# Kernel optimization log

Measured on AMD Instinct MI355X. Metric: run time of the kernel, lower is better.

Reference implementation:

```python
import jax, jax.numpy as jnp
import numpy as np

# segment-boundary byte set (matches ByteContextEncoder.SEGMENT_BYTES)
_SEG_BYTES = b' \t\n\r.,;:!?()[]{}"\'' + b'+-*/=<>|&^~%@#$\\'
_SEP_TABLE = np.zeros(256, dtype=bool)
_SEP_TABLE[list(_SEG_BYTES)] = True

B, T, D, H, L = 4, 2048, 512, 8, 4
HID = 4 * D          # SwiGLU hidden dim
DH = D // H          # head dim
EPS = 1e-6
ALPHA = 0.5
ROPE_BASE = 10000.0


def setup_inputs() -> dict:
    key = jax.random.key(0)
    ks = jax.random.split(key, 10)
    std = D ** -0.5
    tokens = jax.random.randint(ks[0], (B, T), 0, 256)
    embed = jax.random.normal(ks[1], (256, D), dtype=jnp.float32) * std
    wq = jax.random.normal(ks[2], (L, D, D), dtype=jnp.float32) * std
    wk = jax.random.normal(ks[3], (L, D, D), dtype=jnp.float32) * std
    wv = jax.random.normal(ks[4], (L, D, D), dtype=jnp.float32) * std
    wo = jax.random.normal(ks[5], (L, D, D), dtype=jnp.float32) * std
    w1 = jax.random.normal(ks[6], (L, HID, D), dtype=jnp.float32) * std  # gate proj
    w3 = jax.random.normal(ks[7], (L, HID, D), dtype=jnp.float32) * std  # up proj
    w2 = jax.random.normal(ks[8], (L, D, HID), dtype=jnp.float32) * (HID ** -0.5)  # down proj
    attn_norm_w = jnp.ones((L, D), dtype=jnp.float32)
    ffn_norm_w = jnp.ones((L, D), dtype=jnp.float32)
    final_norm_w = jnp.ones((D,), dtype=jnp.float32)
    return {"tokens": tokens, "embed": embed, "attn_norm_w": attn_norm_w,
            "wq": wq, "wk": wk, "wv": wv, "wo": wo,
            "ffn_norm_w": ffn_norm_w, "w1": w1, "w2": w2, "w3": w3,
            "final_norm_w": final_norm_w}


def _rmsnorm(x, w):
    return x * jax.lax.rsqrt(jnp.mean(x * x, axis=-1, keepdims=True) + EPS) * w


def _rope_tables():
    inv = 1.0 / (ROPE_BASE ** (jnp.arange(0, DH, 2, dtype=jnp.float32) / DH))  # (DH/2,)
    ang = jnp.arange(T, dtype=jnp.float32)[:, None] * inv[None, :]             # (T, DH/2)
    return jnp.cos(ang), jnp.sin(ang)


def _apply_rope(x, cos, sin):
    # x: (B, T, H, DH); rotate interleaved pairs
    x1, x2 = x[..., ::2], x[..., 1::2]
    c = cos[None, :, None, :]
    s = sin[None, :, None, :]
    r1 = x1 * c - x2 * s
    r2 = x1 * s + x2 * c
    return jnp.stack([r1, r2], axis=-1).reshape(x.shape)


def _attention(x, Wq, Wk, Wv, Wo, cos, sin):
    q = (x @ Wq.T).reshape(B, T, H, DH)
    k = (x @ Wk.T).reshape(B, T, H, DH)
    v = (x @ Wv.T).reshape(B, T, H, DH)
    q = _apply_rope(q, cos, sin)
    k = _apply_rope(k, cos, sin)
    scores = jnp.einsum('bthd,bshd->bhts', q, k) / jnp.sqrt(jnp.float32(DH))
    a = jax.nn.softmax(scores, axis=-1)  # bidirectional (causal=False)
    o = jnp.einsum('bhts,bshd->bthd', a, v).reshape(B, T, D)
    return o @ Wo.T


def _swiglu(x, W1, W2, W3):
    return (jax.nn.silu(x @ W1.T) * (x @ W3.T)) @ W2.T


def _segment_pool(h, tokens):
    # segment ids via cumsum of separator indicator; per-batch offset b*(T+1)
    sep = jnp.asarray(_SEP_TABLE)[tokens].astype(jnp.int32)          # (B, T)
    seg = jnp.cumsum(sep, axis=1) + jnp.arange(B, dtype=jnp.int32)[:, None] * (T + 1)
    flat_s = seg.reshape(B * T)
    flat_h = h.reshape(B * T, D)
    nseg = B * (T + 1)
    seg_sum = jax.ops.segment_sum(flat_h, flat_s, num_segments=nseg)  # (nseg, D)
    seg_cnt = jax.ops.segment_sum(jnp.ones((B * T,), h.dtype), flat_s, num_segments=nseg)
    seg_cnt = jnp.maximum(seg_cnt, 1.0)
    seg_mean = (seg_sum / seg_cnt[:, None])[flat_s].reshape(B, T, D)
    return ALPHA * h + (1.0 - ALPHA) * seg_mean


def reference(tokens, embed, attn_norm_w, wq, wk, wv, wo, ffn_norm_w, w1, w2, w3, final_norm_w):
    tokens = jnp.clip(tokens, 0, 255)
    x = embed[tokens]  # (B, T, D); dropout=0 -> identity
    cos, sin = _rope_tables()
    for l in range(L):
        x = x + _attention(_rmsnorm(x, attn_norm_w[l]), wq[l], wk[l], wv[l], wo[l], cos, sin)
        x = x + _swiglu(_rmsnorm(x, ffn_norm_w[l]), w1[l], w2[l], w3[l])
    x = _rmsnorm(x, final_norm_w)
    return _segment_pool(x, tokens)
```

## Files before the change

kernel.cpp:

```cpp
#include <hip/hip_runtime.h>
#include <math.h>

#define Bq 4
#define Tt 2048
#define Dd 512
#define Hh 8
#define Ll 4
#define HIDN 2048
#define DHd 64
#define BT (Bq*Tt)
#define BTD ((size_t)BT*Dd)

typedef __attribute__((ext_vector_type(8))) __bf16 bf16x8;
typedef __attribute__((ext_vector_type(4))) __bf16 bf16x4;
typedef __attribute__((ext_vector_type(2))) __bf16 bf16x2;
typedef __attribute__((ext_vector_type(4))) float f32x4;

static __device__ __forceinline__ int is_sep(int t) {
    const unsigned long long w0 = 0xFC00FFFF00002600ULL;
    const unsigned long long w1 = 0x7800000078000001ULL;
    if (t < 64)  return (int)((w0 >> t) & 1ULL);
    if (t < 128) return (int)((w1 >> (t - 64)) & 1ULL);
    return 0;
}

static __device__ __forceinline__ void gload16(const void* g, void* l) {
    __builtin_amdgcn_global_load_lds(
        (const __attribute__((address_space(1))) void*)g,
        (__attribute__((address_space(3))) void*)l, 16, 0, 0);
}

__global__ void embed_kernel(const int* __restrict__ tokens, const float* __restrict__ embed,
                             float* __restrict__ x) {
    size_t idx = (size_t)blockIdx.x * blockDim.x + threadIdx.x;
    if (idx >= BTD / 4) return;
    size_t row = idx >> 7;
    int tk = tokens[row];
    tk = tk < 0 ? 0 : (tk > 255 ? 255 : tk);
    const float4* src = (const float4*)(embed + (size_t)tk * Dd);
    ((float4*)x)[idx] = src[idx & 127];
}

__global__ void rope_table_kernel(float* __restrict__ cosb, float* __restrict__ sinb) {
    int idx = blockIdx.x * blockDim.x + threadIdx.x;
    if (idx >= Tt * 32) return;
    int t = idx >> 5, j = idx & 31;
    float inv = powf(10000.0f, -(2.0f * j) / 64.0f);
    float ang = (float)t * inv;
    cosb[idx] = cosf(ang);
    sinb[idx] = sinf(ang);
}

__global__ void cvt_w_kernel(const float* __restrict__ wo, const float* __restrict__ w1,
                             const float* __restrict__ w3, const float* __restrict__ w2,
                             __bf16* __restrict__ dst) {
    int i = blockIdx.x * blockDim.x + threadIdx.x;
    if (i >= 1703936) return;
    const float* src;
    if (i < 131072)       src = wo + (size_t)i * 8;
    else if (i < 655360)  src = w1 + (size_t)(i - 131072) * 8;
    else if (i < 1179648) src = w3 + (size_t)(i - 655360) * 8;
    else                  src = w2 + (size_t)(i - 1179648) * 8;
    float4 a = *(const float4*)src;
    float4 b = *(const float4*)(src + 4);
    bf16x8 o8;
    o8[0] = (__bf16)a.x; o8[1] = (__bf16)a.y; o8[2] = (__bf16)a.z; o8[3] = (__bf16)a.w;
    o8[4] = (__bf16)b.x; o8[5] = (__bf16)b.y; o8[6] = (__bf16)b.z; o8[7] = (__bf16)b.w;
    *(bf16x8*)(dst + (size_t)i * 8) = o8;
}

__global__ void cvt_qkv_kernel(const float* __restrict__ wq, const float* __restrict__ wk,
                               const float* __restrict__ wv, __bf16* __restrict__ out) {
    int i = blockIdx.x * blockDim.x + threadIdx.x;
    if (i >= 393216) return;
    int l = i / 98304;
    int r = i - l * 98304;
    int t = r >> 15;
    int pos8 = r & 32767;
    const float* src = (t == 0 ? wq : (t == 1 ? wk : wv)) + (size_t)l * 262144 + (size_t)pos8 * 8;
    float4 a = *(const float4*)src;
    float4 b = *(const float4*)(src + 4);
    bf16x8 o8;
    o8[0] = (__bf16)a.x; o8[1] = (__bf16)a.y; o8[2] = (__bf16)a.z; o8[3] = (__bf16)a.w;
    o8[4] = (__bf16)b.x; o8[5] = (__bf16)b.y; o8[6] = (__bf16)b.z; o8[7] = (__bf16)b.w;
    *(bf16x8*)(out + (size_t)i * 8) = o8;
}

__global__ void rmsnorm_bf16_kernel(const float* __restrict__ x, const float* __restrict__ w,
                                    __bf16* __restrict__ y) {
    int row = blockIdx.x * 4 + (threadIdx.x >> 6);
    int lane = threadIdx.x & 63;
    const float* xr = x + (size_t)row * Dd + lane * 8;
    float4 a = *(const float4*)xr;
    float4 b = *(const float4*)(xr + 4);
    float ss = a.x * a.x + a.y * a.y + a.z * a.z + a.w * a.w
             + b.x * b.x + b.y * b.y + b.z * b.z + b.w * b.w;
    #pragma unroll
    for (int off = 1; off < 64; off <<= 1) ss += __shfl_xor(ss, off);
    float scale = rsqrtf(ss * (1.0f / Dd) + 1e-6f);
    const float* wr = w + lane * 8;
    float4 wa = *(const float4*)wr;
    float4 wb = *(const float4*)(wr + 4);
    bf16x8 o;
    o[0] = (__bf16)(a.x * scale * wa.x); o[1] = (__bf16)(a.y * scale * wa.y);
    o[2] = (__bf16)(a.z * scale * wa.z); o[3] = (__bf16)(a.w * scale * wa.w);
    o[4] = (__bf16)(b.x * scale * wb.x); o[5] = (__bf16)(b.y * scale * wb.y);
    o[6] = (__bf16)(b.z * scale * wb.z); o[7] = (__bf16)(b.w * scale * wb.w);
    *(bf16x8*)(y + (size_t)row * Dd + lane * 8) = o;
}

__global__ void rmsnorm_inplace_kernel(float* __restrict__ x, const float* __restrict__ w) {
    int row = blockIdx.x * 4 + (threadIdx.x >> 6);
    int lane = threadIdx.x & 63;
    float* xr = x + (size_t)row * Dd + lane * 8;
    float4 a = *(const float4*)xr;
    float4 b = *(const float4*)(xr + 4);
    float ss = a.x * a.x + a.y * a.y + a.z * a.z + a.w * a.w
             + b.x * b.x + b.y * b.y + b.z * b.z + b.w * b.w;
    #pragma unroll
    for (int off = 1; off < 64; off <<= 1) ss += __shfl_xor(ss, off);
    float scale = rsqrtf(ss * (1.0f / Dd) + 1e-6f);
    const float* wr = w + lane * 8;
    float4 wa = *(const float4*)wr;
    float4 wb = *(const float4*)(wr + 4);
    *(float4*)xr = make_float4(a.x * scale * wa.x, a.y * scale * wa.y,
                               a.z * scale * wa.z, a.w * scale * wa.w);
    *(float4*)(xr + 4) = make_float4(b.x * scale * wb.x, b.y * scale * wb.y,
                                     b.z * scale * wb.z, b.w * scale * wb.w);
}

template<int EPI>
__global__ __launch_bounds__(256) void gemm_bt_mfma(
    const __bf16* __restrict__ A, const __bf16* __restrict__ Bw,
    const float* __restrict__ res, void* __restrict__ Cout,
    int N, int K,
    const float* __restrict__ cosb, const float* __restrict__ sinb) {
    __shared__ __align__(16) __bf16 lds[2][2][128 * 32];
    const int tid = threadIdx.x;
    const int w = tid >> 6, lane = tid & 63;
    const int l15 = lane & 15, g4 = lane >> 4;
    const int wr = w >> 1, wc = w & 1;
    const int bm = blockIdx.y * 128, bn = blockIdx.x * 128;
    const int lrow = lane >> 2, lc8 = (lane & 3) * 8;
    const int chunk0 = w * 2;

    f32x4 acc[4][4];
    #pragma unroll
    for (int m = 0; m < 4; m++)
        #pragma unroll
        for (int n = 0; n < 4; n++) acc[m][n] = (f32x4){0.f, 0.f, 0.f, 0.f};

    auto stage = [&](int buf, int k0) {
        #pragma unroll
        for (int c = 0; c < 2; c++) {
            int chunk = chunk0 + c;
            const __bf16* ga = A + (size_t)(bm + chunk * 16 + lrow) * K + k0 + lc8;
            gload16(ga, &lds[buf][0][chunk * 512]);
            const __bf16* gb = Bw + (size_t)(bn + chunk * 16 + lrow) * K + k0 + lc8;
            gload16(gb, &lds[buf][1][chunk * 512]);
        }
    };

    stage(0, 0);
    __syncthreads();
    const int NT = K >> 5;
    int cur = 0;
    for (int t = 0; t < NT; t++) {
        if (t + 1 < NT) stage(cur ^ 1, (t + 1) << 5);
        const __bf16* Al = &lds[cur][0][0];
        const __bf16* Bl = &lds[cur][1][0];
        bf16x8 af[4], bfr[4];
        #pragma unroll
        for (int m = 0; m < 4; m++)
            af[m] = *(const bf16x8*)&Al[(wr * 64 + m * 16 + l15) * 32 + g4 * 8];
        #pragma unroll
        for (int n = 0; n < 4; n++)
            bfr[n] = *(const bf16x8*)&Bl[(wc * 64 + n * 16 + l15) * 32 + g4 * 8];
        #pragma unroll
        for (int m = 0; m < 4; m++)
            #pragma unroll
            for (int n = 0; n < 4; n++)
                acc[m][n] = __builtin_amdgcn_mfma_f32_16x16x32_bf16(af[m], bfr[n], acc[m][n], 0, 0, 0);
        __syncthreads();
        cur ^= 1;
    }

    #pragma unroll
    for (int m = 0; m < 4; m++)
        #pragma unroll
        for (int n = 0; n < 4; n++)
            #pragma unroll
            for (int r = 0; r < 4; r++) {
                size_t row = bm + wr * 64 + m * 16 + g4 * 4 + r;
                int col = bn + wc * 64 + n * 16 + l15;
                if (EPI == 0) {
                    ((__bf16*)Cout)[row * N + col] = (__bf16)acc[m][n][r];
                } else if (EPI == 1) {
                    ((float*)Cout)[row * N + col] = acc[m][n][r] + res[row * N + col];
                } else {
                    float vv = acc[m][n][r];
                    float vp = __shfl_xor(vv, 1);
                    if (col < 1024) {
                        int trow = (int)(row & (Tt - 1));
                        int p = (col & 63) >> 1;
                        float c = cosb[trow * 32 + p];
                        float s = sinb[trow * 32 + p];
                        float x1 = (col & 1) ? vp : vv;
                        float x2 = (col & 1) ? vv : vp;
                        float rot = (col & 1) ? (x1 * s + x2 * c) : (x1 * c - x2 * s);
                        if (col < 512) rot *= 0.18033688011112043f;
                        vv = rot;
                    }
                    ((__bf16*)Cout)[(size_t)(col >> 9) * BTD + row * 512 + (col & 511)] =
                        (__bf16)vv;
                }
            }
}

__global__ __launch_bounds__(256) void gemm_bt_mfma64(
    const __bf16* __restrict__ A, const __bf16* __restrict__ Bw,
    const float* __restrict__ res, float* __restrict__ Cout,
    int N, int K) {
    __shared__ __align__(16) __bf16 lds[2][2][64 * 32];
    const int tid = threadIdx.x;
    const int w = tid >> 6, lane = tid & 63;
    const int l15 = lane & 15, g4 = lane >> 4;
    const int wr = w >> 1, wc = w & 1;
    const int bm = blockIdx.y * 64, bn = blockIdx.x * 64;
    const int srow = tid >> 2, scol8 = (tid & 3) * 8;

    f32x4 acc[2][2];
    #pragma unroll
    for (int m = 0; m < 2; m++)
        #pragma unroll
        for (int n = 0; n < 2; n++) acc[m][n] = (f32x4){0.f, 0.f, 0.f, 0.f};

    auto stage = [&](int buf, int k0) {
        gload16(A + (size_t)(bm + srow) * K + k0 + scol8, &lds[buf][0][srow * 32 + scol8]);
        gload16(Bw + (size_t)(bn + srow) * K + k0 + scol8, &lds[buf][1][srow * 32 + scol8]);
    };

    stage(0, 0);
    __syncthreads();
    const int NT = K >> 5;
    int cur = 0;
    for (int t = 0; t < NT; t++) {
        if (t + 1 < NT) stage(cur ^ 1, (t + 1) << 5);
        const __bf16* Al = &lds[cur][0][0];
        const __bf16* Bl = &lds[cur][1][0];
        bf16x8 af[2], bfr[2];
        #pragma unroll
        for (int m = 0; m < 2; m++)
            af[m] = *(const bf16x8*)&Al[(wr * 32 + m * 16 + l15) * 32 + g4 * 8];
        #pragma unroll
        for (int n = 0; n < 2; n++)
            bfr[n] = *(const bf16x8*)&Bl[(wc * 32 + n * 16 + l15) * 32 + g4 * 8];
        #pragma unroll
        for (int m = 0; m < 2; m++)
            #pragma unroll
            for (int n = 0; n < 2; n++)
                acc[m][n] = __builtin_amdgcn_mfma_f32_16x16x32_bf16(af[m], bfr[n], acc[m][n], 0, 0, 0);
        __syncthreads();
        cur ^= 1;
    }

    #pragma unroll
    for (int m = 0; m < 2; m++)
        #pragma unroll
        for (int n = 0; n < 2; n++)
            #pragma unroll
            for (int r = 0; r < 4; r++) {
                size_t row = bm + wr * 32 + m * 16 + g4 * 4 + r;
                int col = bn + wc * 32 + n * 16 + l15;
                Cout[row * N + col] = acc[m][n][r] + res[row * N + col];
            }
}

__global__ __launch_bounds__(256) void gemm_swiglu_mfma(
    const __bf16* __restrict__ A, const __bf16* __restrict__ W1,
    const __bf16* __restrict__ W3, __bf16* __restrict__ G,
    int N, int K) {
    __shared__ __align__(16) __bf16 lds[2][3][128 * 32];
    const int tid = threadIdx.x;
    const int w = tid >> 6, lane = tid & 63;
    const int l15 = lane & 15, g4 = lane >> 4;
    const int wr = w >> 1, wc = w & 1;
    const int bm = blockIdx.y * 128, bn = blockIdx.x * 128;
    const int lrow = lane >> 2, lc8 = (lane & 3) * 8;
    const int chunk0 = w * 2;

    f32x4 acc1[4][4], acc3[4][4];
    #pragma unroll
    for (int m = 0; m < 4; m++)
        #pragma unroll
        for (int n = 0; n < 4; n++) {
            acc1[m][n] = (f32x4){0.f, 0.f, 0.f, 0.f};
            acc3[m][n] = (f32x4){0.f, 0.f, 0.f, 0.f};
        }

    auto stage = [&](int buf, int k0) {
        #pragma unroll
        for (int c = 0; c < 2; c++) {
            int chunk = chunk0 + c;
            const __bf16* ga = A + (size_t)(bm + chunk * 16 + lrow) * K + k0 + lc8;
            gload16(ga, &lds[buf][0][chunk * 512]);
            const __bf16* g1 = W1 + (size_t)(bn + chunk * 16 + lrow) * K + k0 + lc8;
            gload16(g1, &lds[buf][1][chunk * 512]);
            const __bf16* g3 = W3 + (size_t)(bn + chunk * 16 + lrow) * K + k0 + lc8;
            gload16(g3, &lds[buf][2][chunk * 512]);
        }
    };

    stage(0, 0);
    __syncthreads();
    const int NT = K >> 5;
    int cur = 0;
    for (int t = 0; t < NT; t++) {
        if (t + 1 < NT) stage(cur ^ 1, (t + 1) << 5);
        const __bf16* Al = &lds[cur][0][0];
        const __bf16* B1 = &lds[cur][1][0];
        const __bf16* B3 = &lds[cur][2][0];
        bf16x8 af[4];
        #pragma unroll
        for (int m = 0; m < 4; m++)
            af[m] = *(const bf16x8*)&Al[(wr * 64 + m * 16 + l15) * 32 + g4 * 8];
        #pragma unroll
        for (int n = 0; n < 4; n++) {
            bf16x8 b1 = *(const bf16x8*)&B1[(wc * 64 + n * 16 + l15) * 32 + g4 * 8];
            bf16x8 b3 = *(const bf16x8*)&B3[(wc * 64 + n * 16 + l15) * 32 + g4 * 8];
            #pragma unroll
            for (int m = 0; m < 4; m++) {
                acc1[m][n] = __builtin_amdgcn_mfma_f32_16x16x32_bf16(af[m], b1, acc1[m][n], 0, 0, 0);
                acc3[m][n] = __builtin_amdgcn_mfma_f32_16x16x32_bf16(af[m], b3, acc3[m][n], 0, 0, 0);
            }
        }
        __syncthreads();
        cur ^= 1;
    }

    #pragma unroll
    for (int m = 0; m < 4; m++)
        #pragma unroll
        for (int n = 0; n < 4; n++)
            #pragma unroll
            for (int r = 0; r < 4; r++) {
                size_t row = bm + wr * 64 + m * 16 + g4 * 4 + r;
                size_t col = bn + wc * 64 + n * 16 + l15;
                float a1 = acc1[m][n][r];
                float sig = 1.0f / (1.0f + __expf(-a1));
                G[row * N + col] = (__bf16)(a1 * sig * acc3[m][n][r]);
            }
}

__global__ __launch_bounds__(512) void attn_mfma_kernel(
    const __bf16* __restrict__ q, const __bf16* __restrict__ k,
    const __bf16* __restrict__ v, __bf16* __restrict__ o) {
    __shared__ __align__(16) __bf16 Ks[2][64][72];
    __shared__ __align__(16) unsigned int VtW[2][64 * 36];

    int tid = threadIdx.x;
    int w = tid >> 6;
    int lane = tid & 63;
    int l15 = lane & 15;
    int g = lane >> 4;
    int i = blockIdx.x;
    int xcd = i & 7, jj = i >> 3;
    int bh = xcd * 4 + (jj >> 4);
    int qtile = jj & 15;
    int b = bh >> 3, h = bh & 7;
    int qbase = qtile * 128;

    const __bf16* qp = q + (size_t)b * Tt * Dd + (size_t)h * DHd;
    const __bf16* kp = k + (size_t)b * Tt * Dd + (size_t)h * DHd;
    const __bf16* vp = v + (size_t)b * Tt * Dd + (size_t)h * DHd;

    int krow = tid >> 3;
    int ksc8 = (tid & 7) * 8;
    int r2v  = tid >> 4;
    int sc4  = (tid & 15) * 4;
    int sgrow = 8 * (l15 >> 2) + (l15 & 3);

    bf16x8 qa[2];
    {
        const __bf16* qrow = qp + (size_t)(qbase + w * 16 + l15) * Dd;
        qa[0] = *(const bf16x8*)(qrow + g * 8);
        qa[1] = *(const bf16x8*)(qrow + 32 + g * 8);
    }

    f32x4 oacc[4];
    #pragma unroll
    for (int i2 = 0; i2 < 4; i2++) oacc[i2] = (f32x4){0.f, 0.f, 0.f, 0.f};
    float mrun = -1e30f;
    float lrun = 0.f;

    bf16x8 kreg;
    bf16x4 vreg0, vreg1;
    auto ldkv = [&](int t) {
        size_t base = (size_t)(t * 64) * Dd;
        kreg  = *(const bf16x8*)(kp + base + (size_t)krow * Dd + ksc8);
        vreg0 = *(const bf16x4*)(vp + base + (size_t)(2 * r2v) * Dd + sc4);
        vreg1 = *(const bf16x4*)(vp + base + (size_t)(2 * r2v + 1) * Dd + sc4);
    };
    auto stash = [&](int buf) {
        *(bf16x8*)&Ks[buf][krow][ksc8] = kreg;
        const unsigned short* v0 = (const unsigned short*)&vreg0;
        const unsigned short* v1 = (const unsigned short*)&vreg1;
        #pragma unroll
        for (int j = 0; j < 4; j++) {
            int d = sc4 + j;
            int col = (r2v + 4 * ((d >> 3) & 7)) & 31;
            unsigned int word = (unsigned int)v0[j] | ((unsigned int)v1[j] << 16);
            VtW[buf][d * 36 + col] = word;
        }
    };

    const int NT = Tt / 64;
    ldkv(0);
    stash(0);
    ldkv(1);
    __syncthreads();

    for (int t = 0; t < NT; t++) {
        int cur = t & 1;
        f32x4 s4[4];
        __builtin_amdgcn_s_setprio(1);
        #pragma unroll
        for (int c = 0; c < 4; c++) {
            int row = sgrow + (c & 1) * 32 + (c >> 1) * 4;
            s4[c] = (f32x4){0.f, 0.f, 0.f, 0.f};
            bf16x8 kb0 = *(const bf16x8*)&Ks[cur][row][g * 8];
            s4[c] = __builtin_amdgcn_mfma_f32_16x16x32_bf16(kb0, qa[0], s4[c], 0, 0, 0);
            bf16x8 kb1 = *(const bf16x8*)&Ks[cur][row][32 + g * 8];
            s4[c] = __builtin_amdgcn_mfma_f32_16x16x32_bf16(kb1, qa[1], s4[c], 0, 0, 0);
        }
        __builtin_amdgcn_s_setprio(0);

        if (t + 1 < NT) stash(cur ^ 1);
        if (t + 2 < NT) ldkv(t + 2);

        float lm = fmaxf(fmaxf(fmaxf(s4[0][0], s4[0][1]), fmaxf(s4[0][2], s4[0][3])),
                         fmaxf(fmaxf(s4[1][0], s4[1][1]), fmaxf(s4[1][2], s4[1][3])));
        lm = fmaxf(lm, fmaxf(fmaxf(s4[2][0], s4[2][1]), fmaxf(s4[2][2], s4[2][3])));
        lm = fmaxf(lm, fmaxf(fmaxf(s4[3][0], s4[3][1]), fmaxf(s4[3][2], s4[3][3])));
        bool near = (lm - mrun <= 8.f);
        if (!__all((int)near)) {
            float tm = fmaxf(lm, __shfl_xor(lm, 16));
            tm = fmaxf(tm, __shfl_xor(tm, 32));
            float mnew = fmaxf(mrun, tm);
            float alpha = exp2f(mrun - mnew);
            mrun = mnew;
            lrun *= alpha;
            float ar[4];
            #pragma unroll
            for (int r = 0; r < 4; r++) ar[r] = __shfl(alpha, 20 * g + r);
            #pragma unroll
            for (int d2 = 0; d2 < 4; d2++)
                #pragma unroll
                for (int r = 0; r < 4; r++) oacc[d2][r] *= ar[r];
        }
        float psum = 0.f;
        bf16x8 pa0, pa1;
        #pragma unroll
        for (int cc = 0; cc < 2; cc++)
            #pragma unroll
            for (int r = 0; r < 4; r++) {
                float e0 = exp2f(s4[2 * cc][r] - mrun);
                float e1 = exp2f(s4[2 * cc + 1][r] - mrun);
                psum += e0 + e1;
                pa0[cc * 4 + r] = (__bf16)e0;
                pa1[cc * 4 + r] = (__bf16)e1;
            }
        lrun += psum;

        __builtin_amdgcn_s_setprio(1);
        #pragma unroll
        for (int d2 = 0; d2 < 4; d2++) {
            int d = d2 * 16 + l15;
            int rot = ((2 * d2 + (l15 >> 3)) & 7) * 4;
            const unsigned int* vrow = VtW[cur] + d * 36;
            bf16x8 vb0 = *(const bf16x8*)(vrow + ((4 * g + rot) & 31));
            bf16x8 vb1 = *(const bf16x8*)(vrow + ((16 + 4 * g + rot) & 31));
            oacc[d2] = __builtin_amdgcn_mfma_f32_16x16x32_bf16(pa0, vb0, oacc[d2], 0, 0, 0);
            oacc[d2] = __builtin_amdgcn_mfma_f32_16x16x32_bf16(pa1, vb1, oacc[d2], 0, 0, 0);
        }
        __builtin_amdgcn_s_setprio(0);

        __syncthreads();
    }

    lrun += __shfl_xor(lrun, 16);
    lrun += __shfl_xor(lrun, 32);
    float lr[4];
    #pragma unroll
    for (int r = 0; r < 4; r++) lr[r] = __shfl(lrun, 20 * g + r);

    __bf16* op = o + (size_t)b * Tt * Dd + (size_t)h * DHd;
    #pragma unroll
    for (int d2 = 0; d2 < 4; d2++)
        #pragma unroll
        for (int r = 0; r < 4; r++)
            op[(size_t)(qbase + w * 16 + g * 4 + r) * Dd + d2 * 16 + l15] =
                (__bf16)(oacc[d2][r] / lr[r]);
}

__global__ void seg_scan_kernel(const int* __restrict__ tokens, int* __restrict__ segid,
                                float* __restrict__ cnt) {
    int b = blockIdx.x;
    int tid = threadIdx.x;
    const int* trow = tokens + (size_t)b * Tt;
    int base = tid * 8;
    int inc[8];
    int run = 0;
    #pragma unroll
    for (int i = 0; i < 8; i++) {
        int tk = trow[base + i];
        tk = tk < 0 ? 0 : (tk > 255 ? 255 : tk);
        run += is_sep(tk);
        inc[i] = run;
    }
    __shared__ int part[256];
    part[tid] = run;
    __syncthreads();
    for (int off = 1; off < 256; off <<= 1) {
        int vv = (tid >= off) ? part[tid - off] : 0;
        __syncthreads();
        part[tid] += vv;
        __syncthreads();
    }
    int exc = part[tid] - run;
    int sid[8];
    #pragma unroll
    for (int i = 0; i < 8; i++) {
        sid[i] = exc + inc[i] + b * (Tt + 1);
        segid[(size_t)b * Tt + base + i] = sid[i];
    }
    int curid = sid[0];
    float c = 1.0f;
    #pragma unroll
    for (int i = 1; i < 8; i++) {
        if (sid[i] == curid) c += 1.0f;
        else { atomicAdd(&cnt[curid], c); curid = sid[i]; c = 1.0f; }
    }
    atomicAdd(&cnt[curid], c);
}

__global__ void seg_accum_kernel(const float* __restrict__ h, const int* __restrict__ segid,
                                 float* __restrict__ segsum) {
    size_t idx = (size_t)blockIdx.x * blockDim.x + threadIdx.x;
    if (idx >= BTD) return;
    size_t row = idx >> 9;
    int d = idx & 511;
    atomicAdd(&segsum[(size_t)segid[row] * Dd + d], h[idx]);
}

__global__ void seg_final_kernel(const float* __restrict__ h, const float* __restrict__ segsum,
                                 const float* __restrict__ cnt, const int* __restrict__ segid,
                                 float* __restrict__ out) {
    size_t idx = (size_t)blockIdx.x * blockDim.x + threadIdx.x;
    if (idx >= BTD) return;
    size_t row = idx >> 9;
    int d = idx & 511;
    int s = segid[row];
    float mean = segsum[(size_t)s * Dd + d] / fmaxf(cnt[s], 1.0f);
    out[idx] = 0.5f * h[idx] + 0.5f * mean;
}

extern "C" void kernel_launch(void* const* d_in, const int* in_sizes, int n_in,
                              void* d_out, int out_size, void* d_ws, size_t ws_size,
                              hipStream_t stream) {
    const int*   tokens       = (const int*)d_in[0];
    const float* embedw       = (const float*)d_in[1];
    const float* attn_norm_w  = (const float*)d_in[2];
    const float* wq           = (const float*)d_in[3];
    const float* wk           = (const float*)d_in[4];
    const float* wv           = (const float*)d_in[5];
    const float* wo           = (const float*)d_in[6];
    const float* ffn_norm_w   = (const float*)d_in[7];
    const float* w1           = (const float*)d_in[8];
    const float* w2           = (const float*)d_in[9];
    const float* w3           = (const float*)d_in[10];
    const float* final_norm_w = (const float*)d_in[11];
    float* out = (float*)d_out;
    float* ws  = (float*)d_ws;

    float*  x    = ws;
    __bf16* qkvo = (__bf16*)(ws + BTD);
    __bf16* qb   = qkvo;
    __bf16* kb   = qkvo + BTD;
    __bf16* vb   = qkvo + 2 * BTD;
    __bf16* obuf = qkvo + 3 * BTD;
    __bf16* gbuf = qkvo;
    float*  segsum = ws + BTD;
    __bf16* xnb  = (__bf16*)(ws + 3 * BTD);
    __bf16* wb   = (__bf16*)(ws + 3 * BTD + BTD / 2);
    float*  cosb = ws + 3 * BTD + BTD / 2 + 8388608;
    float*  sinb = cosb + (size_t)Tt * 32;
    float*  segcnt = sinb + (size_t)Tt * 32;
    int*    segid  = (int*)(segcnt + Bq * (Tt + 1));

    __bf16* wqkvb = wb;
    __bf16* wob = wb + 3145728;
    __bf16* w1b = wb + 4194304;
    __bf16* w3b = wb + 8388608;
    __bf16* w2b = wb + 12582912;

    cvt_qkv_kernel<<<1536, 256, 0, stream>>>(wq, wk, wv, wqkvb);
    cvt_w_kernel<<<6656, 256, 0, stream>>>(wo, w1, w3, w2, wob);

    embed_kernel<<<(int)((BTD / 4 + 255) / 256), 256, 0, stream>>>(tokens, embedw, x);
    rope_table_kernel<<<(Tt * 32 + 255) / 256, 256, 0, stream>>>(cosb, sinb);

    dim3 gqkv(12, 64);
    dim3 g64(8, 128);
    dim3 gs(16, 64);
    dim3 ga(512);
    int grms = BT / 4;

    for (int l = 0; l < Ll; l++) {
        size_t oDD = (size_t)l * Dd * Dd;
        size_t oHD = (size_t)l * HIDN * Dd;
        rmsnorm_bf16_kernel<<<grms, 256, 0, stream>>>(x, attn_norm_w + (size_t)l * Dd, xnb);
        gemm_bt_mfma<2><<<gqkv, 256, 0, stream>>>(xnb, wqkvb + (size_t)l * 786432, nullptr, qb,
                                                  1536, Dd, cosb, sinb);
        attn_mfma_kernel<<<ga, 512, 0, stream>>>(qb, kb, vb, obuf);
        gemm_bt_mfma64<<<g64, 256, 0, stream>>>(obuf, wob + oDD, x, x, Dd, Dd);
        rmsnorm_bf16_kernel<<<grms, 256, 0, stream>>>(x, ffn_norm_w + (size_t)l * Dd, xnb);
        gemm_swiglu_mfma<<<gs, 256, 0, stream>>>(xnb, w1b + oHD, w3b + oHD, gbuf, HIDN, Dd);
        gemm_bt_mfma64<<<g64, 256, 0, stream>>>(gbuf, w2b + oHD, x, x, Dd, HIDN);
    }

    rmsnorm_inplace_kernel<<<grms, 256, 0, stream>>>(x, final_norm_w);
    hipMemsetAsync(segsum, 0, (size_t)Bq * (Tt + 1) * Dd * sizeof(float), stream);
    hipMemsetAsync(segcnt, 0, (size_t)Bq * (Tt + 1) * sizeof(float), stream);
    seg_scan_kernel<<<Bq, 256, 0, stream>>>(tokens, segid, segcnt);
    seg_accum_kernel<<<(int)((BTD + 255) / 256), 256, 0, stream>>>(x, segid, segsum);
    seg_final_kernel<<<(int)((BTD + 255) / 256), 256, 0, stream>>>(x, segsum, segcnt, segid, out);
}
```

Before: 972.0 us.

## Use 128x128 split-K GEMM with atomic accumulation for FFN down projection

Replaces the 64x64-tile down-projection GEMM (K=2048) with a dedicated 128x128-tile kernel that splits K into four 512-wide slices across grid z. Each block adds its partial result straight into the residual x with float atomicAdd, which also performs the residual add. The larger tiles raise MFMA reuse per LDS load and split-K keeps 1024 blocks in flight. The cost is atomic traffic on x and a summation order that is no longer deterministic.

```diff
diff --git a/kernel.cpp b/kernel.cpp
--- a/kernel.cpp
+++ b/kernel.cpp
@@ -217,6 +217,72 @@
             }
 }
 
+__global__ __launch_bounds__(256) void gemm_w2_splitk(
+    const __bf16* __restrict__ A, const __bf16* __restrict__ Bw,
+    float* __restrict__ Cout) {
+    __shared__ __align__(16) __bf16 lds[2][2][128 * 32];
+    const int tid = threadIdx.x;
+    const int w = tid >> 6, lane = tid & 63;
+    const int l15 = lane & 15, g4 = lane >> 4;
+    const int wr = w >> 1, wc = w & 1;
+    const int bm = blockIdx.y * 128, bn = blockIdx.x * 128;
+    const int kz = blockIdx.z * 512;
+    const int lrow = lane >> 2, lc8 = (lane & 3) * 8;
+    const int chunk0 = w * 2;
+
+    f32x4 acc[4][4];
+    #pragma unroll
+    for (int m = 0; m < 4; m++)
+        #pragma unroll
+        for (int n = 0; n < 4; n++) acc[m][n] = (f32x4){0.f, 0.f, 0.f, 0.f};
+
+    auto stage = [&](int buf, int k0) {
+        #pragma unroll
+        for (int c = 0; c < 2; c++) {
+            int chunk = chunk0 + c;
+            const __bf16* ga = A + (size_t)(bm + chunk * 16 + lrow) * HIDN + kz + k0 + lc8;
+            gload16(ga, &lds[buf][0][chunk * 512]);
+            const __bf16* gb = Bw + (size_t)(bn + chunk * 16 + lrow) * HIDN + kz + k0 + lc8;
+            gload16(gb, &lds[buf][1][chunk * 512]);
+        }
+    };
+
+    stage(0, 0);
+    __syncthreads();
+    const int NT = 512 >> 5;
+    int cur = 0;
+    for (int t = 0; t < NT; t++) {
+        if (t + 1 < NT) stage(cur ^ 1, (t + 1) << 5);
+        const __bf16* Al = &lds[cur][0][0];
+        const __bf16* Bl = &lds[cur][1][0];
+        bf16x8 af[4], bfr[4];
+        #pragma unroll
+        for (int m = 0; m < 4; m++)
+            af[m] = *(const bf16x8*)&Al[(wr * 64 + m * 16 + l15) * 32 + g4 * 8];
+        #pragma unroll
+        for (int n = 0; n < 4; n++)
+            bfr[n] = *(const bf16x8*)&Bl[(wc * 64 + n * 16 + l15) * 32 + g4 * 8];
+        #pragma unroll
+        for (int m = 0; m < 4; m++)
+            #pragma unroll
+            for (int n = 0; n < 4; n++)
+                acc[m][n] = __builtin_amdgcn_mfma_f32_16x16x32_bf16(af[m], bfr[n], acc[m][n], 0, 0, 0);
+        __syncthreads();
+        cur ^= 1;
+    }
+
+    #pragma unroll
+    for (int m = 0; m < 4; m++)
+        #pragma unroll
+        for (int n = 0; n < 4; n++)
+            #pragma unroll
+            for (int r = 0; r < 4; r++) {
+                size_t row = bm + wr * 64 + m * 16 + g4 * 4 + r;
+                int col = bn + wc * 64 + n * 16 + l15;
+                atomicAdd(&Cout[row * Dd + col], acc[m][n][r]);
+            }
+}
+
 __global__ __launch_bounds__(256) void gemm_bt_mfma64(
     const __bf16* __restrict__ A, const __bf16* __restrict__ Bw,
     const float* __restrict__ res, float* __restrict__ Cout,
@@ -613,6 +679,7 @@
     dim3 gqkv(12, 64);
     dim3 g64(8, 128);
     dim3 gs(16, 64);
+    dim3 gw2(4, 64, 4);
     dim3 ga(512);
     int grms = BT / 4;
 
@@ -626,7 +693,7 @@
         gemm_bt_mfma64<<<g64, 256, 0, stream>>>(obuf, wob + oDD, x, x, Dd, Dd);
         rmsnorm_bf16_kernel<<<grms, 256, 0, stream>>>(x, ffn_norm_w + (size_t)l * Dd, xnb);
         gemm_swiglu_mfma<<<gs, 256, 0, stream>>>(xnb, w1b + oHD, w3b + oHD, gbuf, HIDN, Dd);
-        gemm_bt_mfma64<<<g64, 256, 0, stream>>>(gbuf, w2b + oHD, x, x, Dd, HIDN);
+        gemm_w2_splitk<<<gw2, 256, 0, stream>>>(gbuf, w2b + oHD, x);
     }
 
     rmsnorm_inplace_kernel<<<grms, 256, 0, stream>>>(x, final_norm_w);
```

Measured after the change: 1.068 ms. 1.1x slower.
